# Kernel optimization log

Hardware: AMD Instinct MI355X
Metric: run time of the kernel (lower is better)

The kernel has to match this reference:

```python
import jax, jax.numpy as jnp
import numpy as np

B, S, D, H = 4, 2048, 1024, 16
HD = D // H
NEG = -1000000.0  # matches sequence_mask fill value in the torch source


def setup_inputs() -> dict:
    key = jax.random.key(0)
    kq, kk, kv, kl, k1, k2, k3, k4 = jax.random.split(key, 8)
    scale = 1.0 / np.sqrt(D)
    return {
        "queries": jax.random.normal(kq, (B, S, D), dtype=jnp.float32),
        "keys": jax.random.normal(kk, (B, S, D), dtype=jnp.float32),
        "values": jax.random.normal(kv, (B, S, D), dtype=jnp.float32),
        "valid_lens": jax.random.randint(kl, (B,), 0, S, dtype=jnp.int64),
        "Wq": jax.random.normal(k1, (D, D), dtype=jnp.float32) * scale,
        "Wk": jax.random.normal(k2, (D, D), dtype=jnp.float32) * scale,
        "Wv": jax.random.normal(k3, (D, D), dtype=jnp.float32) * scale,
        "Wo": jax.random.normal(k4, (D, D), dtype=jnp.float32) * scale,
    }


def reference(queries, keys, values, valid_lens, Wq, Wk, Wv, Wo):
    def split_heads(x):  # [B,S,D] -> [B,H,S,HD]
        return x.reshape(B, S, H, HD).transpose(0, 2, 1, 3)

    q = split_heads(queries @ Wq)
    k = split_heads(keys @ Wk)
    v = split_heads(values @ Wv)

    scores = jnp.einsum("bhqd,bhkd->bhqk", q, k) / np.sqrt(HD)
    # padding mask over key positions: key index < valid_len[b]
    key_mask = jnp.arange(S)[None, :] < valid_lens[:, None]  # [B,S]
    scores = jnp.where(key_mask[:, None, None, :], scores, NEG)
    attn = jax.nn.softmax(scores, axis=-1)
    # dropout p=0.0 -> identity
    out = jnp.einsum("bhqk,bhkd->bhqd", attn, v)
    out = out.transpose(0, 2, 1, 3).reshape(B, S, D)  # merge heads
    return out @ Wo
```

## Files before the change

### kernel.cpp

```cpp
#include <hip/hip_runtime.h>
#include <hip/hip_bf16.h>

#define B_ 4
#define S_ 2048
#define D_ 1024
#define H_ 16
#define HD_ 64
#define M_ 8192
#define NEGV -1000000.0f
#define CEXP 0.18033688011112042f

typedef __attribute__((ext_vector_type(8))) __bf16 bf16x8;
typedef __attribute__((ext_vector_type(4))) float f32x4;
typedef __attribute__((ext_vector_type(16))) float f32x16;

__device__ __forceinline__ f32x4 mfma16(bf16x8 a, bf16x8 b, f32x4 c) {
  return __builtin_amdgcn_mfma_f32_16x16x32_bf16(a, b, c, 0, 0, 0);
}
__device__ __forceinline__ f32x16 mfma32(bf16x8 a, bf16x8 b, f32x16 c) {
  return __builtin_amdgcn_mfma_f32_32x32x16_bf16(a, b, c, 0, 0, 0);
}

#if __has_builtin(__builtin_amdgcn_exp2f)
__device__ __forceinline__ float exp2_hw(float x) { return __builtin_amdgcn_exp2f(x); }
#else
__device__ __forceinline__ float exp2_hw(float x) {
  float r;
  asm volatile("v_exp_f32 %0, %1" : "=v"(r) : "v"(x));
  return r;
}
#endif

__device__ __forceinline__ unsigned bf16rz(float x) {
  unsigned u = __float_as_uint(x);
  return (u + 0x7FFFu + ((u >> 16) & 1u)) >> 16;
}
__device__ __forceinline__ unsigned pk2bf(float a, float b) {
  unsigned ua = __float_as_uint(a), ub = __float_as_uint(b);
  ua = ua + 0x7FFFu + ((ua >> 16) & 1u);
  ub = ub + 0x7FFFu + ((ub >> 16) & 1u);
  return (ua >> 16) | (ub & 0xFFFF0000u);
}

__device__ __forceinline__ void gld_lds16(const __hip_bfloat16* g, __hip_bfloat16* l) {
  __builtin_amdgcn_global_load_lds(
      (const __attribute__((address_space(1))) void*)g,
      (__attribute__((address_space(3))) void*)l, 16, 0, 0);
}

__global__ __launch_bounds__(256) void convert_x(const float* __restrict__ X,
                                                 __hip_bfloat16* __restrict__ Y, int n4,
                                                 const int* __restrict__ vskip) {
  int i = blockIdx.x * blockDim.x + threadIdx.x;
  if (i >= n4) return;
  if (vskip) {
    int gm = i >> 8;
    int vlen = vskip[gm >> 11];
    if (vlen > 0 && (gm & 2047) >= ((vlen + 63) & ~63)) return;
  }
  float4 v = reinterpret_cast<const float4*>(X)[i];
  uint2 o;
  o.x = pk2bf(v.x, v.y);
  o.y = pk2bf(v.z, v.w);
  reinterpret_cast<uint2*>(Y)[i] = o;
}

__global__ __launch_bounds__(256) void convert_wt4(const float* __restrict__ W0,
                                                   const float* __restrict__ W1,
                                                   const float* __restrict__ W2,
                                                   const float* __restrict__ W3,
                                                   __hip_bfloat16* __restrict__ WtBase) {
  const int z = blockIdx.z;
  const float* W = (z == 0) ? W0 : (z == 1) ? W1 : (z == 2) ? W2 : W3;
  __hip_bfloat16* Wt = WtBase + (size_t)z * D_ * D_;
  __shared__ float tile[32][33];
  int c0 = blockIdx.x * 32, r0 = blockIdx.y * 32;
  int tx = threadIdx.x, ty = threadIdx.y;
#pragma unroll
  for (int rr = ty; rr < 32; rr += 8)
    tile[rr][tx] = W[(size_t)(r0 + rr) * D_ + c0 + tx];
  __syncthreads();
#pragma unroll
  for (int rr = ty; rr < 32; rr += 8)
    reinterpret_cast<unsigned short*>(Wt)[(size_t)(c0 + rr) * D_ + r0 + tx] =
        (unsigned short)bf16rz(tile[tx][rr]);
}

template <int EPI>
__global__ __launch_bounds__(256) void gemm_bt(const __hip_bfloat16* __restrict__ A,
                                               const __hip_bfloat16* __restrict__ Bt,
                                               void* __restrict__ Cout,
                                               const int* __restrict__ vskip,
                                               float cscale) {
  int id = blockIdx.y * gridDim.x + blockIdx.x;
  int cpx = (gridDim.x * gridDim.y) >> 3;
  int nid = (id & 7) * cpx + (id >> 3);
  const int m0 = (nid >> 3) * 128, n0 = (nid & 7) * 128;
  if (vskip) {
    int vlen = vskip[m0 >> 11];
    if (vlen > 0 && (m0 & 2047) >= ((vlen + 63) & ~63)) return;
  }
  const int t = threadIdx.x, lane = t & 63, wid = t >> 6;
  const int lc = lane & 15, g = lane >> 4;
  const int srow8 = lane >> 3, sg8 = lane & 7;
  __shared__ __align__(16) __hip_bfloat16 smem[2][2][128 * 64];
  f32x4 acc[4][4] = {};
  const int wm = (wid & 1) * 64, wn = (wid >> 1) * 64;

  auto stage = [&](int buf, int k0) {
#pragma unroll
    for (int c = 0; c < 4; ++c) {
      int ci = c * 4 + wid;
      int row = ci * 8 + srow8;
      int sg = sg8 ^ (row & 7);
      gld_lds16(A + (size_t)(m0 + row) * D_ + k0 + sg * 8, &smem[buf][0][ci * 512]);
      gld_lds16(Bt + (size_t)(n0 + row) * D_ + k0 + sg * 8, &smem[buf][1][ci * 512]);
    }
  };

  stage(0, 0);
  asm volatile("s_waitcnt vmcnt(0)" ::: "memory");
  __syncthreads();
  int cur = 0;

  for (int kt = 0; kt < D_ / 64; ++kt) {
    if (kt + 1 < D_ / 64) stage(cur ^ 1, (kt + 1) * 64);
    const __hip_bfloat16* As = smem[cur][0];
    const __hip_bfloat16* Bs = smem[cur][1];
#pragma unroll
    for (int kh = 0; kh < 2; ++kh) {
      bf16x8 af[4], bf[4];
#pragma unroll
      for (int mi = 0; mi < 4; ++mi) {
        int r = wm + mi * 16 + lc;
        af[mi] = *reinterpret_cast<const bf16x8*>(
            As + r * 64 + (((kh * 4 + g) ^ (r & 7)) << 3));
        int rn = wn + mi * 16 + lc;
        bf[mi] = *reinterpret_cast<const bf16x8*>(
            Bs + rn * 64 + (((kh * 4 + g) ^ (rn & 7)) << 3));
      }
#pragma unroll
      for (int mi = 0; mi < 4; ++mi)
#pragma unroll
        for (int ni = 0; ni < 4; ++ni)
          acc[mi][ni] = mfma16(af[mi], bf[ni], acc[mi][ni]);
    }
    asm volatile("s_waitcnt vmcnt(0)" ::: "memory");
    __syncthreads();
    cur ^= 1;
  }

#pragma unroll
  for (int mi = 0; mi < 4; ++mi) {
#pragma unroll
    for (int ni = 0; ni < 4; ++ni) {
#pragma unroll
      for (int i = 0; i < 4; ++i) {
        int gm = m0 + wm + mi * 16 + g * 4 + i;
        int gn = n0 + wn + ni * 16 + lc;
        float val = acc[mi][ni][i] * cscale;
        if constexpr (EPI == 0) {
          int b = gm >> 11, s = gm & 2047, h = gn >> 6, d = gn & 63;
          reinterpret_cast<unsigned short*>(
              Cout)[(((size_t)(b * H_ + h) * S_ + s) << 6) + d] =
              (unsigned short)bf16rz(val);
        } else if constexpr (EPI == 1) {
          int b = gm >> 11, s = gm & 2047, h = gn >> 6, d = gn & 63;
          reinterpret_cast<unsigned short*>(
              Cout)[(((size_t)(b * H_ + h) * HD_ + d) << 11) + s] =
              (unsigned short)bf16rz(val);
        } else {
          ((float*)Cout)[(size_t)gm * D_ + gn] = val;
        }
      }
    }
  }
}

__global__ __launch_bounds__(256) void attn(const __hip_bfloat16* __restrict__ Qh,
                                            const __hip_bfloat16* __restrict__ Kh,
                                            const __hip_bfloat16* __restrict__ Vt,
                                            const int* __restrict__ vlens,
                                            __hip_bfloat16* __restrict__ O,
                                            int* __restrict__ ctr) {
  const int t = threadIdx.x, lane = t & 63, w = t >> 6;
  const int q = lane & 31;
  const int hh = lane >> 5;

  int va = vlens[0], vb = vlens[1], vc = vlens[2], vd = vlens[3];
  int ia = 0, ib = 1, ic = 2, id_ = 3;
  {
    int tv, ti;
#define CSWAP(x, xi, y, yi) \
    if (y > x) { tv = x; x = y; y = tv; ti = xi; xi = yi; yi = ti; }
    CSWAP(va, ia, vb, ib) CSWAP(vc, ic, vd, id_)
    CSWAP(va, ia, vc, ic) CSWAP(vb, ib, vd, id_)
    CSWAP(vb, ib, vc, ic)
#undef CSWAP
  }
  __shared__ int s_unit;
  __shared__ __align__(16) __hip_bfloat16 smem[3][8192];

  while (true) {
    if (t == 0) s_unit = atomicAdd(ctr, 1);
    __syncthreads();
    const int u = s_unit;
    if (u >= 1024) break;
    const int rank = u >> 8;
    const int b = (rank == 0) ? ia : (rank == 1) ? ib : (rank == 2) ? ic : id_;
    const int vlen = (rank == 0) ? va : (rank == 1) ? vb : (rank == 2) ? vc : vd;
    const int r = u & 255;
    const int h = r & 15, qt = r >> 4;
    const int bh = b * 16 + h;

    const __hip_bfloat16* Qb = Qh + (size_t)bh * S_ * HD_;
    const __hip_bfloat16* Kb = Kh + (size_t)bh * S_ * HD_;
    const __hip_bfloat16* Vb = Vt + (size_t)bh * HD_ * S_;

    const int qrow = qt * 128 + w * 32 + q;
    bf16x8 qf[4];
#pragma unroll
    for (int kk = 0; kk < 4; ++kk)
      qf[kk] = *reinterpret_cast<const bf16x8*>(Qb + (size_t)qrow * HD_ + kk * 16 + hh * 8);

    f32x16 accT[2] = {};
    float l_half = 0.f;

    const int srow = lane >> 3;
    const int sg = lane & 7;
    const float maskv = (vlen == 0) ? 0.f : NEGV;
    const int kv_end = (vlen == 0) ? S_ : min(S_, (vlen + 63) & ~63);
    const int nt = kv_end >> 6;

    auto stage = [&](int buf, int tile) {
      int kv = tile * 64;
#pragma unroll
      for (int c = 0; c < 2; ++c) {
        int rr = w * 16 + c * 8 + srow;
        int gs = sg ^ (rr & 7);
        gld_lds16(Kb + (size_t)(kv + rr) * HD_ + gs * 8, smem[buf] + (w * 16 + c * 8) * 64);
        gld_lds16(Vb + (size_t)rr * S_ + kv + gs * 8,
                  smem[buf] + 4096 + (w * 16 + c * 8) * 64);
      }
    };

    stage(0, 0);
    if (nt > 1) stage(1, 1);
    int bc = 0;
    int bs = (nt > 2) ? 2 : 0;

    for (int tt = 0; tt < nt; ++tt) {
      if (tt + 1 < nt) {
        asm volatile("s_waitcnt vmcnt(4)" ::: "memory");
      } else {
        asm volatile("s_waitcnt vmcnt(0)" ::: "memory");
      }
      __syncthreads();
      if (tt + 2 < nt) stage(bs, tt + 2);

      const __hip_bfloat16* Ks = smem[bc];
      const __hip_bfloat16* Vs = smem[bc] + 4096;

      f32x16 sc[2];
#pragma unroll
      for (int ct = 0; ct < 2; ++ct) {
        f32x16 a = {};
#pragma unroll
        for (int kk = 0; kk < 4; ++kk) {
          int row = ct * 32 + q;
          bf16x8 kf = *reinterpret_cast<const bf16x8*>(
              Ks + row * 64 + (((kk * 2 + hh) ^ (row & 7)) << 3));
          a = mfma32(kf, qf[kk], a);
        }
        sc[ct] = a;
      }

      int kv = tt * 64;
      if (kv + 64 > vlen) {
#pragma unroll
        for (int ct = 0; ct < 2; ++ct)
#pragma unroll
          for (int rr = 0; rr < 16; ++rr) {
            int j = kv + ct * 32 + (rr & 3) + 8 * (rr >> 2) + 4 * hh;
            if (j >= vlen) sc[ct][rr] = maskv;
          }
      }

      uint wlo[8], whi[8];
      float rs = 0.f;
#pragma unroll
      for (int a2 = 0; a2 < 8; ++a2) {
        float p0 = exp2_hw(sc[a2 >> 2][(a2 & 3) * 4 + 0]);
        float p1 = exp2_hw(sc[a2 >> 2][(a2 & 3) * 4 + 1]);
        float p2 = exp2_hw(sc[a2 >> 2][(a2 & 3) * 4 + 2]);
        float p3 = exp2_hw(sc[a2 >> 2][(a2 & 3) * 4 + 3]);
        rs += (p0 + p1) + (p2 + p3);
        wlo[a2] = pk2bf(p0, p1);
        whi[a2] = pk2bf(p2, p3);
      }
      l_half += rs;

#pragma unroll
      for (int kk = 0; kk < 4; ++kk) {
        uint glo = wlo[2 * kk], ghi = whi[2 * kk];
        uint flo = wlo[2 * kk + 1], fhi = whi[2 * kk + 1];
        uint slo = hh ? glo : flo, shi = hh ? ghi : fhi;
        uint rlo = __shfl_xor(slo, 32), rhi = __shfl_xor(shi, 32);
        union { uint u[4]; bf16x8 v; } pf;
        pf.u[0] = hh ? rlo : glo;
        pf.u[1] = hh ? rhi : ghi;
        pf.u[2] = hh ? flo : rlo;
        pf.u[3] = hh ? fhi : rhi;
#pragma unroll
        for (int ctd = 0; ctd < 2; ++ctd) {
          int vr = ctd * 32 + q;
          bf16x8 vf = *reinterpret_cast<const bf16x8*>(
              Vs + vr * 64 + (((kk * 2 + hh) ^ (vr & 7)) << 3));
          accT[ctd] = mfma32(vf, pf.v, accT[ctd]);
        }
      }
      bc = (bc == 2) ? 0 : bc + 1;
      bs = (bs == 2) ? 0 : bs + 1;
    }
    __syncthreads();

    float l_tot = l_half + __shfl_xor(l_half, 32);
    float inv = 1.f / l_tot;
    __hip_bfloat16* Ot = smem[0] + w * 2048;
#pragma unroll
    for (int ctd = 0; ctd < 2; ++ctd)
#pragma unroll
      for (int a2 = 0; a2 < 4; ++a2) {
        uint2 o;
        o.x = pk2bf(accT[ctd][a2 * 4 + 0] * inv, accT[ctd][a2 * 4 + 1] * inv);
        o.y = pk2bf(accT[ctd][a2 * 4 + 2] * inv, accT[ctd][a2 * 4 + 3] * inv);
        int gs8 = (ctd * 8 + a2 * 2 + hh) ^ ((q & 7) << 1);
        *reinterpret_cast<uint2*>(Ot + q * 64 + gs8 * 4) = o;
      }
#pragma unroll
    for (int rr = 0; rr < 4; ++rr) {
      int row = rr * 8 + (lane >> 3);
      int c16 = lane & 7;
      float4 v4 = *reinterpret_cast<const float4*>(
          Ot + row * 64 + (((c16 * 2) ^ ((row & 7) << 1)) << 2));
      int s = qt * 128 + w * 32 + row;
      *reinterpret_cast<float4*>(O + ((size_t)b * S_ + s) * D_ + h * HD_ + c16 * 8) = v4;
    }
  }
}

extern "C" void kernel_launch(void* const* d_in, const int* in_sizes, int n_in,
                              void* d_out, int out_size, void* d_ws, size_t ws_size,
                              hipStream_t stream) {
  const float* Xq = (const float*)d_in[0];
  const float* Xk = (const float*)d_in[1];
  const float* Xv = (const float*)d_in[2];
  const int* vl = (const int*)d_in[3];
  const float* Wq = (const float*)d_in[4];
  const float* Wk = (const float*)d_in[5];
  const float* Wv = (const float*)d_in[6];
  const float* Wo = (const float*)d_in[7];
  float* out = (float*)d_out;

  char* ws = (char*)d_ws;
  const size_t XB = (size_t)M_ * D_ * 2;
  const size_t WB = (size_t)D_ * D_ * 2;
  __hip_bfloat16* xb = (__hip_bfloat16*)(ws);
  __hip_bfloat16* wtq = (__hip_bfloat16*)(ws + XB);
  __hip_bfloat16* wtk = (__hip_bfloat16*)(ws + XB + WB);
  __hip_bfloat16* wtv = (__hip_bfloat16*)(ws + XB + 2 * WB);
  __hip_bfloat16* wto = (__hip_bfloat16*)(ws + XB + 3 * WB);
  __hip_bfloat16* Qh = (__hip_bfloat16*)(ws + XB + 4 * WB);
  __hip_bfloat16* Kh = (__hip_bfloat16*)(ws + 2 * XB + 4 * WB);
  __hip_bfloat16* Vh = (__hip_bfloat16*)(ws + 3 * XB + 4 * WB);
  __hip_bfloat16* Obuf = xb;
  int* ctr = (int*)wtv;

  convert_wt4<<<dim3(32, 32, 4), dim3(32, 8), 0, stream>>>(Wq, Wk, Wv, Wo, wtq);

  const int n4 = M_ * D_ / 4;
  dim3 gg(M_ / 128, D_ / 128);
  convert_x<<<n4 / 256, 256, 0, stream>>>(Xq, xb, n4, nullptr);
  gemm_bt<0><<<gg, 256, 0, stream>>>(xb, wtq, Qh, nullptr, CEXP);
  convert_x<<<n4 / 256, 256, 0, stream>>>(Xk, xb, n4, vl);
  gemm_bt<0><<<gg, 256, 0, stream>>>(xb, wtk, Kh, vl, 1.0f);
  convert_x<<<n4 / 256, 256, 0, stream>>>(Xv, xb, n4, vl);
  gemm_bt<1><<<gg, 256, 0, stream>>>(xb, wtv, Vh, vl, 1.0f);

  hipMemsetAsync(ctr, 0, sizeof(int), stream);
  attn<<<dim3(1024), 256, 0, stream>>>(Qh, Kh, Vh, vl, Obuf, ctr);
  gemm_bt<2><<<gg, 256, 0, stream>>>(Obuf, wto, out, nullptr, 1.0f);
}
```

Baseline: 211.8 us.

## Split KV range of longest-batch attention units across two workgroups

Attention work units for the batches with the longest valid lengths, taken in sorted order, are split into two halves over the KV tile range. Each half writes fp32 partial accumulators and row sums to a workspace slot, and the second half to arrive (detected via an atomic flag) merges them and writes the normalized output. This targets load imbalance at the tail of the persistent scheduler, where long-sequence units otherwise dominate. It costs extra global traffic for partials, an extra memset, and fence/atomic synchronization. The split is enabled only if the workspace is large enough.

```diff
diff --git a/kernel.cpp b/kernel.cpp
--- a/kernel.cpp
+++ b/kernel.cpp
@@ -182,7 +182,10 @@
                                             const __hip_bfloat16* __restrict__ Vt,
                                             const int* __restrict__ vlens,
                                             __hip_bfloat16* __restrict__ O,
-                                            int* __restrict__ ctr) {
+                                            int* __restrict__ ctr,
+                                            float* __restrict__ part,
+                                            int* __restrict__ flags,
+                                            int split_u) {
   const int t = threadIdx.x, lane = t & 63, w = t >> 6;
   const int q = lane & 31;
   const int hh = lane >> 5;
@@ -198,18 +201,25 @@
     CSWAP(vb, ib, vc, ic)
 #undef CSWAP
   }
+  const int nsub = (split_u >> 1) + 1024;
   __shared__ int s_unit;
+  __shared__ int s_arr;
   __shared__ __align__(16) __hip_bfloat16 smem[3][8192];
 
   while (true) {
     if (t == 0) s_unit = atomicAdd(ctr, 1);
     __syncthreads();
     const int u = s_unit;
-    if (u >= 1024) break;
-    const int rank = u >> 8;
+    if (u >= nsub) break;
+    int rank, r, sub, issplit;
+    if (u < split_u) {
+      rank = u >> 9; int rr = u & 511; sub = rr & 1; r = rr >> 1; issplit = 1;
+    } else {
+      int v = u - split_u; rank = (split_u >> 9) + (v >> 8); r = v & 255;
+      sub = 0; issplit = 0;
+    }
     const int b = (rank == 0) ? ia : (rank == 1) ? ib : (rank == 2) ? ic : id_;
     const int vlen = (rank == 0) ? va : (rank == 1) ? vb : (rank == 2) ? vc : vd;
-    const int r = u & 255;
     const int h = r & 15, qt = r >> 4;
     const int bh = b * 16 + h;
 
@@ -230,7 +240,14 @@
     const int sg = lane & 7;
     const float maskv = (vlen == 0) ? 0.f : NEGV;
     const int kv_end = (vlen == 0) ? S_ : min(S_, (vlen + 63) & ~63);
-    const int nt = kv_end >> 6;
+    const int nt_total = kv_end >> 6;
+    int tb0 = 0, tb1 = nt_total;
+    if (issplit) {
+      int nth = (nt_total + 1) >> 1;
+      tb0 = sub * nth;
+      tb1 = min(nt_total, tb0 + nth);
+    }
+    const int nloc = tb1 - tb0;
 
     auto stage = [&](int buf, int tile) {
       int kv = tile * 64;
@@ -244,107 +261,148 @@
       }
     };
 
-    stage(0, 0);
-    if (nt > 1) stage(1, 1);
-    int bc = 0;
-    int bs = (nt > 2) ? 2 : 0;
-
-    for (int tt = 0; tt < nt; ++tt) {
-      if (tt + 1 < nt) {
-        asm volatile("s_waitcnt vmcnt(4)" ::: "memory");
+    if (nloc > 0) {
+      stage(0, tb0);
+      if (nloc > 1) stage(1, tb0 + 1);
+      int bc = 0;
+      int bs = (nloc > 2) ? 2 : 0;
+
+      for (int i = 0; i < nloc; ++i) {
+        if (i + 1 < nloc) {
+          asm volatile("s_waitcnt vmcnt(4)" ::: "memory");
+        } else {
+          asm volatile("s_waitcnt vmcnt(0)" ::: "memory");
+        }
+        __syncthreads();
+        if (i + 2 < nloc) stage(bs, tb0 + i + 2);
+
+        const __hip_bfloat16* Ks = smem[bc];
+        const __hip_bfloat16* Vs = smem[bc] + 4096;
+
+        f32x16 sc[2];
+#pragma unroll
+        for (int ct = 0; ct < 2; ++ct) {
+          f32x16 a = {};
+#pragma unroll
+          for (int kk = 0; kk < 4; ++kk) {
+            int row = ct * 32 + q;
+            bf16x8 kf = *reinterpret_cast<const bf16x8*>(
+                Ks + row * 64 + (((kk * 2 + hh) ^ (row & 7)) << 3));
+            a = mfma32(kf, qf[kk], a);
+          }
+          sc[ct] = a;
+        }
+
+        int kv = (tb0 + i) * 64;
+        if (kv + 64 > vlen) {
+#pragma unroll
+          for (int ct = 0; ct < 2; ++ct)
+#pragma unroll
+            for (int rr = 0; rr < 16; ++rr) {
+              int j = kv + ct * 32 + (rr & 3) + 8 * (rr >> 2) + 4 * hh;
+              if (j >= vlen) sc[ct][rr] = maskv;
+            }
+        }
+
+        uint wlo[8], whi[8];
+        float rs = 0.f;
+#pragma unroll
+        for (int a2 = 0; a2 < 8; ++a2) {
+          float p0 = exp2_hw(sc[a2 >> 2][(a2 & 3) * 4 + 0]);
+          float p1 = exp2_hw(sc[a2 >> 2][(a2 & 3) * 4 + 1]);
+          float p2 = exp2_hw(sc[a2 >> 2][(a2 & 3) * 4 + 2]);
+          float p3 = exp2_hw(sc[a2 >> 2][(a2 & 3) * 4 + 3]);
+          rs += (p0 + p1) + (p2 + p3);
+          wlo[a2] = pk2bf(p0, p1);
+          whi[a2] = pk2bf(p2, p3);
+        }
+        l_half += rs;
+
+#pragma unroll
+        for (int kk = 0; kk < 4; ++kk) {
+          uint glo = wlo[2 * kk], ghi = whi[2 * kk];
+          uint flo = wlo[2 * kk + 1], fhi = whi[2 * kk + 1];
+          uint slo = hh ? glo : flo, shi = hh ? ghi : fhi;
+          uint rlo = __shfl_xor(slo, 32), rhi = __shfl_xor(shi, 32);
+          union { uint u[4]; bf16x8 v; } pf;
+          pf.u[0] = hh ? rlo : glo;
+          pf.u[1] = hh ? rhi : ghi;
+          pf.u[2] = hh ? flo : rlo;
+          pf.u[3] = hh ? fhi : rhi;
+#pragma unroll
+          for (int ctd = 0; ctd < 2; ++ctd) {
+            int vr = ctd * 32 + q;
+            bf16x8 vf = *reinterpret_cast<const bf16x8*>(
+                Vs + vr * 64 + (((kk * 2 + hh) ^ (vr & 7)) << 3));
+            accT[ctd] = mfma32(vf, pf.v, accT[ctd]);
+          }
+        }
+        bc = (bc == 2) ? 0 : bc + 1;
+        bs = (bs == 2) ? 0 : bs + 1;
+      }
+    }
+    __syncthreads();
+
+    bool do_out = true;
+    if (issplit) {
+      const int punit = (rank << 8) | r;
+      float* slot = part + ((size_t)(punit * 2 + sub) * 1024 + (w * 64 + lane)) * 36;
+#pragma unroll
+      for (int ctd = 0; ctd < 2; ++ctd)
+#pragma unroll
+        for (int a2 = 0; a2 < 4; ++a2) {
+          float4 v4 = make_float4(accT[ctd][a2 * 4 + 0], accT[ctd][a2 * 4 + 1],
+                                  accT[ctd][a2 * 4 + 2], accT[ctd][a2 * 4 + 3]);
+          reinterpret_cast<float4*>(slot)[ctd * 4 + a2] = v4;
+        }
+      slot[32] = l_half;
+      __threadfence();
+      __syncthreads();
+      if (t == 0) s_arr = atomicAdd(&flags[punit], 1);
+      __syncthreads();
+      if (s_arr == 0) {
+        do_out = false;
       } else {
-        asm volatile("s_waitcnt vmcnt(0)" ::: "memory");
-      }
-      __syncthreads();
-      if (tt + 2 < nt) stage(bs, tt + 2);
-
-      const __hip_bfloat16* Ks = smem[bc];
-      const __hip_bfloat16* Vs = smem[bc] + 4096;
-
-      f32x16 sc[2];
-#pragma unroll
-      for (int ct = 0; ct < 2; ++ct) {
-        f32x16 a = {};
-#pragma unroll
-        for (int kk = 0; kk < 4; ++kk) {
-          int row = ct * 32 + q;
-          bf16x8 kf = *reinterpret_cast<const bf16x8*>(
-              Ks + row * 64 + (((kk * 2 + hh) ^ (row & 7)) << 3));
-          a = mfma32(kf, qf[kk], a);
-        }
-        sc[ct] = a;
-      }
-
-      int kv = tt * 64;
-      if (kv + 64 > vlen) {
-#pragma unroll
-        for (int ct = 0; ct < 2; ++ct)
-#pragma unroll
-          for (int rr = 0; rr < 16; ++rr) {
-            int j = kv + ct * 32 + (rr & 3) + 8 * (rr >> 2) + 4 * hh;
-            if (j >= vlen) sc[ct][rr] = maskv;
+        __threadfence();
+        const float* ps = part + ((size_t)(punit * 2 + (sub ^ 1)) * 1024 +
+                                  (w * 64 + lane)) * 36;
+#pragma unroll
+        for (int ctd = 0; ctd < 2; ++ctd)
+#pragma unroll
+          for (int a2 = 0; a2 < 4; ++a2) {
+            float4 v4 = reinterpret_cast<const float4*>(ps)[ctd * 4 + a2];
+            accT[ctd][a2 * 4 + 0] += v4.x;
+            accT[ctd][a2 * 4 + 1] += v4.y;
+            accT[ctd][a2 * 4 + 2] += v4.z;
+            accT[ctd][a2 * 4 + 3] += v4.w;
           }
-      }
-
-      uint wlo[8], whi[8];
-      float rs = 0.f;
-#pragma unroll
-      for (int a2 = 0; a2 < 8; ++a2) {
-        float p0 = exp2_hw(sc[a2 >> 2][(a2 & 3) * 4 + 0]);
-        float p1 = exp2_hw(sc[a2 >> 2][(a2 & 3) * 4 + 1]);
-        float p2 = exp2_hw(sc[a2 >> 2][(a2 & 3) * 4 + 2]);
-        float p3 = exp2_hw(sc[a2 >> 2][(a2 & 3) * 4 + 3]);
-        rs += (p0 + p1) + (p2 + p3);
-        wlo[a2] = pk2bf(p0, p1);
-        whi[a2] = pk2bf(p2, p3);
-      }
-      l_half += rs;
-
-#pragma unroll
-      for (int kk = 0; kk < 4; ++kk) {
-        uint glo = wlo[2 * kk], ghi = whi[2 * kk];
-        uint flo = wlo[2 * kk + 1], fhi = whi[2 * kk + 1];
-        uint slo = hh ? glo : flo, shi = hh ? ghi : fhi;
-        uint rlo = __shfl_xor(slo, 32), rhi = __shfl_xor(shi, 32);
-        union { uint u[4]; bf16x8 v; } pf;
-        pf.u[0] = hh ? rlo : glo;
-        pf.u[1] = hh ? rhi : ghi;
-        pf.u[2] = hh ? flo : rlo;
-        pf.u[3] = hh ? fhi : rhi;
-#pragma unroll
-        for (int ctd = 0; ctd < 2; ++ctd) {
-          int vr = ctd * 32 + q;
-          bf16x8 vf = *reinterpret_cast<const bf16x8*>(
-              Vs + vr * 64 + (((kk * 2 + hh) ^ (vr & 7)) << 3));
-          accT[ctd] = mfma32(vf, pf.v, accT[ctd]);
-        }
-      }
-      bc = (bc == 2) ? 0 : bc + 1;
-      bs = (bs == 2) ? 0 : bs + 1;
-    }
-    __syncthreads();
-
-    float l_tot = l_half + __shfl_xor(l_half, 32);
-    float inv = 1.f / l_tot;
-    __hip_bfloat16* Ot = smem[0] + w * 2048;
-#pragma unroll
-    for (int ctd = 0; ctd < 2; ++ctd)
-#pragma unroll
-      for (int a2 = 0; a2 < 4; ++a2) {
-        uint2 o;
-        o.x = pk2bf(accT[ctd][a2 * 4 + 0] * inv, accT[ctd][a2 * 4 + 1] * inv);
-        o.y = pk2bf(accT[ctd][a2 * 4 + 2] * inv, accT[ctd][a2 * 4 + 3] * inv);
-        int gs8 = (ctd * 8 + a2 * 2 + hh) ^ ((q & 7) << 1);
-        *reinterpret_cast<uint2*>(Ot + q * 64 + gs8 * 4) = o;
-      }
-#pragma unroll
-    for (int rr = 0; rr < 4; ++rr) {
-      int row = rr * 8 + (lane >> 3);
-      int c16 = lane & 7;
-      float4 v4 = *reinterpret_cast<const float4*>(
-          Ot + row * 64 + (((c16 * 2) ^ ((row & 7) << 1)) << 2));
-      int s = qt * 128 + w * 32 + row;
-      *reinterpret_cast<float4*>(O + ((size_t)b * S_ + s) * D_ + h * HD_ + c16 * 8) = v4;
+        l_half += ps[32];
+      }
+    }
+
+    if (do_out) {
+      float l_tot = l_half + __shfl_xor(l_half, 32);
+      float inv = 1.f / l_tot;
+      __hip_bfloat16* Ot = smem[0] + w * 2048;
+#pragma unroll
+      for (int ctd = 0; ctd < 2; ++ctd)
+#pragma unroll
+        for (int a2 = 0; a2 < 4; ++a2) {
+          uint2 o;
+          o.x = pk2bf(accT[ctd][a2 * 4 + 0] * inv, accT[ctd][a2 * 4 + 1] * inv);
+          o.y = pk2bf(accT[ctd][a2 * 4 + 2] * inv, accT[ctd][a2 * 4 + 3] * inv);
+          int gs8 = (ctd * 8 + a2 * 2 + hh) ^ ((q & 7) << 1);
+          *reinterpret_cast<uint2*>(Ot + q * 64 + gs8 * 4) = o;
+        }
+#pragma unroll
+      for (int rr = 0; rr < 4; ++rr) {
+        int row = rr * 8 + (lane >> 3);
+        int c16 = lane & 7;
+        float4 v4 = *reinterpret_cast<const float4*>(
+            Ot + row * 64 + (((c16 * 2) ^ ((row & 7) << 1)) << 2));
+        int s = qt * 128 + w * 32 + row;
+        *reinterpret_cast<float4*>(O + ((size_t)b * S_ + s) * D_ + h * HD_ + c16 * 8) = v4;
+      }
     }
   }
 }
@@ -376,6 +434,14 @@
   __hip_bfloat16* Obuf = xb;
   int* ctr = (int*)wtv;
 
+  const size_t BASE = 4 * XB + 4 * WB;
+  int* flags = (int*)(ws + BASE);
+  float* part = (float*)(ws + BASE + 4096);
+  const size_t slot_bytes = (size_t)1024 * 36 * 4;
+  const size_t need2 = BASE + 4096 + 512 * 2 * slot_bytes;
+  const size_t need1 = BASE + 4096 + 256 * 2 * slot_bytes;
+  const int split_u = (ws_size >= need2) ? 1024 : (ws_size >= need1 ? 512 : 0);
+
   convert_wt4<<<dim3(32, 32, 4), dim3(32, 8), 0, stream>>>(Wq, Wk, Wv, Wo, wtq);
 
   const int n4 = M_ * D_ / 4;
@@ -388,6 +454,7 @@
   gemm_bt<1><<<gg, 256, 0, stream>>>(xb, wtv, Vh, vl, 1.0f);
 
   hipMemsetAsync(ctr, 0, sizeof(int), stream);
-  attn<<<dim3(1024), 256, 0, stream>>>(Qh, Kh, Vh, vl, Obuf, ctr);
+  if (split_u) hipMemsetAsync(flags, 0, 4096, stream);
+  attn<<<dim3(1024), 256, 0, stream>>>(Qh, Kh, Vh, vl, Obuf, ctr, part, flags, split_u);
   gemm_bt<2><<<gg, 256, 0, stream>>>(Obuf, wto, out, nullptr, 1.0f);
 }
```

After: 447.3 us. +111.2%, slower.
